# Optimization experiments

Hardware: AMD Instinct MI355X
Metric: run time of the kernel (lower is better)

The kernel has to match this reference:

```python
import jax, jax.numpy as jnp
import numpy as np

H = 56; W = 56; WS = 7; SHIFT = 3; HEADS = 6; C = 192
HD = C // HEADS; N = WS * WS; NWH = H // WS; NWW = W // WS; NW = NWH * NWW
MLP_HID = 4 * C
EPS = 1e-5


def _rel_index(ws):
    coords = np.stack(np.meshgrid(np.arange(ws), np.arange(ws), indexing='ij'))  # [2,ws,ws]
    cf = coords.reshape(2, -1)                       # [2,N]
    rc = (cf[:, :, None] - cf[:, None, :]).transpose(1, 2, 0).astype(np.int64)  # [N,N,2]
    rc[..., 0] += ws - 1
    rc[..., 1] += ws - 1
    rc[..., 0] *= 2 * ws - 1
    return rc.sum(-1)                                # [N,N]


def _attn_mask(h, w, ws, shift):
    img = np.zeros((h, w), dtype=np.float32)
    slices = (slice(0, -ws), slice(-ws, -shift), slice(-shift, None))
    cnt = 0
    for hs in slices:
        for wsl in slices:
            img[hs, wsl] = cnt
            cnt += 1
    mw = img.reshape(h // ws, ws, w // ws, ws).transpose(0, 2, 1, 3).reshape(-1, ws * ws)  # [nW,N]
    am = mw[:, None, :] - mw[:, :, None]             # [nW,N,N] (unsqueeze(1)-unsqueeze(2))
    return np.where(am != 0, np.float32(-100.0), np.float32(0.0))


REL_IDX = jnp.asarray(_rel_index(WS))
ATTN_MASK = jnp.asarray(_attn_mask(H, W, WS, SHIFT))


def _ln(x, w, b):
    m = jnp.mean(x, axis=-1, keepdims=True)
    v = jnp.mean((x - m) ** 2, axis=-1, keepdims=True)
    return (x - m) * jax.lax.rsqrt(v + EPS) * w + b


def setup_inputs() -> dict:
    key = jax.random.key(0)
    ks = jax.random.split(key, 8)
    B = 64
    s = 0.02
    return {
        'x': jax.random.normal(ks[0], (B, H * W, C), jnp.float32),
        'norm1_w': jnp.ones((C,), jnp.float32),
        'norm1_b': jnp.zeros((C,), jnp.float32),
        'qkv_w': jax.random.normal(ks[1], (C, 3 * C), jnp.float32) * s,
        'qkv_b': jnp.zeros((3 * C,), jnp.float32),
        'proj_w': jax.random.normal(ks[2], (C, C), jnp.float32) * s,
        'proj_b': jnp.zeros((C,), jnp.float32),
        'rel_bias': jax.random.normal(ks[3], ((2 * WS - 1) ** 2, HEADS), jnp.float32) * s,
        'norm2_w': jnp.ones((C,), jnp.float32),
        'norm2_b': jnp.zeros((C,), jnp.float32),
        'fc1_w': jax.random.normal(ks[4], (C, MLP_HID), jnp.float32) * s,
        'fc1_b': jnp.zeros((MLP_HID,), jnp.float32),
        'fc2_w': jax.random.normal(ks[5], (MLP_HID, C), jnp.float32) * s,
        'fc2_b': jnp.zeros((C,), jnp.float32),
    }


def reference(x, norm1_w, norm1_b, qkv_w, qkv_b, proj_w, proj_b, rel_bias,
              norm2_w, norm2_b, fc1_w, fc1_b, fc2_w, fc2_b):
    B = x.shape[0]
    shortcut = x
    h = _ln(x, norm1_w, norm1_b).reshape(B, H, W, C)
    h = jnp.roll(h, (-SHIFT, -SHIFT), axis=(1, 2))
    # window partition -> [B*nW, N, C]
    wx = h.reshape(B, NWH, WS, NWW, WS, C).transpose(0, 1, 3, 2, 4, 5).reshape(B * NW, N, C)
    qkv = (wx @ qkv_w + qkv_b).reshape(B * NW, N, 3, HEADS, HD).transpose(2, 0, 3, 1, 4)
    q, k, v = qkv[0], qkv[1], qkv[2]                 # [BnW, heads, N, hd]
    attn = jnp.einsum('bhnd,bhmd->bhnm', q, k) * (HD ** -0.5)
    bias = rel_bias[REL_IDX.reshape(-1)].reshape(N, N, HEADS).transpose(2, 0, 1)  # [heads,N,N]
    attn = attn + bias[None]
    attn = attn.reshape(B, NW, HEADS, N, N) + ATTN_MASK[None, :, None]
    attn = jax.nn.softmax(attn.reshape(B * NW, HEADS, N, N), axis=-1)
    out = jnp.einsum('bhnm,bhmd->bhnd', attn, v).transpose(0, 2, 1, 3).reshape(B * NW, N, C)
    out = out @ proj_w + proj_b
    # window reverse -> [B,H,W,C]
    out = out.reshape(B, NWH, NWW, WS, WS, C).transpose(0, 1, 3, 2, 4, 5).reshape(B, H, W, C)
    out = jnp.roll(out, (SHIFT, SHIFT), axis=(1, 2)).reshape(B, H * W, C)
    x = shortcut + out
    h2 = _ln(x, norm2_w, norm2_b)
    h2 = jax.nn.gelu(h2 @ fc1_w + fc1_b, approximate=False)
    h2 = h2 @ fc2_w + fc2_b
    return x + h2
```

## Files before the change

kernel.cpp:

```cpp
#include <hip/hip_runtime.h>
#include <hip/hip_bf16.h>
#include <math.h>

typedef __bf16 bf16;
typedef bf16  bf16x4 __attribute__((ext_vector_type(4)));
typedef bf16  bf16x8 __attribute__((ext_vector_type(8)));
typedef float f32x4  __attribute__((ext_vector_type(4)));

#define CD 192
#define NHEADS 6

__device__ __forceinline__ bf16x8 ld_frag(const bf16* p, int r0, int k0, int ld) {
  const int l = threadIdx.x & 63;
  return *reinterpret_cast<const bf16x8*>(p + (r0 + (l & 15)) * ld + (k0 + 8 * (l >> 4)));
}

__device__ __forceinline__ f32x4 mfma16(bf16x8 a, bf16x8 b, f32x4 c) {
  return __builtin_amdgcn_mfma_f32_16x16x32_bf16(a, b, c, 0, 0, 0);
}

__device__ __forceinline__ float gelu_f(float v) {
  const float e = __expf(-1.5957691216057308f * (v + 0.044715f * v * v * v));
  return v * __builtin_amdgcn_rcpf(1.f + e);
}

__global__ void prep_pack(const float* __restrict__ src, bf16* __restrict__ dst, int K, int N) {
  const int t = blockIdx.x * 256 + threadIdx.x;
  const int ktiles = K >> 5;
  const int total = (N >> 4) * ktiles * 64;
  if (t >= total) return;
  const int l  = t & 63;
  const int r  = t >> 6;
  const int kt = r % ktiles;
  const int ng = r / ktiles;
  const int n  = ng * 16 + (l & 15);
  const int k0 = kt * 32 + 8 * (l >> 4);
  bf16x8 v;
  #pragma unroll
  for (int j = 0; j < 8; ++j) v[j] = (bf16)src[(size_t)(k0 + j) * N + n];
  *(reinterpret_cast<bf16x8*>(dst) + t) = v;
}

__global__ void prep_bm(const float* __restrict__ relb, float* __restrict__ bm) {
  const int idx = blockIdx.x * 256 + threadIdx.x;
  if (idx >= 4 * 6 * 64 * 64) return;
  const int k = idx & 63;
  const int r = (idx >> 6) & 63;
  const int h = (idx >> 12) % 6;
  const int c = idx / (4096 * 6);
  float v = -3000.f;
  if (r < 49 && k < 49) {
    const int rh = r / 7, rw = r % 7, kh = k / 7, kw = k % 7;
    const int crh = (c & 2) ? (rh < 4 ? 1 : 2) : 0;
    const int crw = (c & 1) ? (rw < 4 ? 1 : 2) : 0;
    const int ckh = (c & 2) ? (kh < 4 ? 1 : 2) : 0;
    const int ckw = (c & 1) ? (kw < 4 ? 1 : 2) : 0;
    const float mask = (crh == ckh && crw == ckw) ? 0.f : -100.f;
    v = relb[((rh - kh + 6) * 13 + (rw - kw + 6)) * 6 + h] + mask;
  }
  bm[idx] = v;
}

__global__ __launch_bounds__(768, 1)
void swin_attn_kernel(const float* __restrict__ x,
                      const float* __restrict__ n1w, const float* __restrict__ n1b,
                      const bf16* __restrict__ wqf, const float* __restrict__ qkvb,
                      const bf16* __restrict__ wpf, const float* __restrict__ projb,
                      const float* __restrict__ bm,
                      float* __restrict__ out)
{
  __shared__ alignas(16) bf16 sQ[NHEADS][64 * 40];
  __shared__ alignas(16) bf16 sK[NHEADS][64 * 40];
  __shared__ alignas(16) bf16 sVT[NHEADS][32 * 72];
  __shared__ alignas(16) bf16 sU[NHEADS * 64 * 72];

  const int l    = threadIdx.x & 63;
  const int wv   = threadIdx.x >> 6;
  const int h    = wv >> 1;
  const int half = wv & 1;
  const int r0w  = half * 32;
  const int b  = blockIdx.x >> 6;
  const int wi = blockIdx.x & 63;
  const int wh = wi >> 3, ww = wi & 7;
  const int cw = ((wh == 7) ? 2 : 0) + ((ww == 7) ? 1 : 0);

  bf16* sA = sU;

  {
    const float w0 = n1w[l], w1 = n1w[l + 64], w2 = n1w[l + 128];
    const float c0 = n1b[l], c1 = n1b[l + 64], c2 = n1b[l + 128];
    float v0a[5], v1a[5], v2a[5];
    #pragma unroll
    for (int it = 0; it < 5; ++it) {
      const int t = wv + it * 12;
      if (t < 49) {
        const int th = t / 7, tw = t - 7 * th;
        const int ho = (wh * 7 + th + 3) % 56;
        const int wo = (ww * 7 + tw + 3) % 56;
        const float* xr = x + ((size_t)b * 3136 + ho * 56 + wo) * CD;
        v0a[it] = xr[l]; v1a[it] = xr[l + 64]; v2a[it] = xr[l + 128];
      }
    }
    #pragma unroll
    for (int it = 0; it < 5; ++it) {
      const int t = wv + it * 12;
      if (t < 49) {
        const float v0 = v0a[it], v1 = v1a[it], v2 = v2a[it];
        float s  = v0 + v1 + v2;
        float ss = v0 * v0 + v1 * v1 + v2 * v2;
        #pragma unroll
        for (int off = 32; off; off >>= 1) { s += __shfl_xor(s, off); ss += __shfl_xor(ss, off); }
        const float mean = s * (1.f / 192.f);
        const float inv  = rsqrtf(ss * (1.f / 192.f) - mean * mean + 1e-5f);
        sA[t * 200 + l]       = (bf16)((v0 - mean) * inv * w0 + c0);
        sA[t * 200 + l + 64]  = (bf16)((v1 - mean) * inv * w1 + c1);
        sA[t * 200 + l + 128] = (bf16)((v2 - mean) * inv * w2 + c2);
      }
    }
    for (int i = threadIdx.x; i < 15 * 200; i += 768) sA[49 * 200 + i] = (bf16)0.f;
  }
  __syncthreads();

  float bmreg[2][4][4];
  {
    const float* bmb = bm + ((size_t)(cw * 6 + h) << 12) + (l & 15);
    #pragma unroll
    for (int mt = 0; mt < 2; ++mt)
      #pragma unroll
      for (int i = 0; i < 4; ++i) {
        const int r = r0w + mt * 16 + (l >> 4) * 4 + i;
        #pragma unroll
        for (int nt = 0; nt < 4; ++nt)
          bmreg[mt][i][nt] = bmb[r * 64 + nt * 16];
      }
  }

  {
    const bf16x8* bq = reinterpret_cast<const bf16x8*>(wqf) + l;
    f32x4 acc[6][2] = {};
    #pragma unroll
    for (int ks = 0; ks < 6; ++ks) {
      const int k0 = ks * 32;
      bf16x8 af0 = ld_frag(sA, r0w,      k0, 200);
      bf16x8 af1 = ld_frag(sA, r0w + 16, k0, 200);
      #pragma unroll
      for (int nt = 0; nt < 6; ++nt) {
        const int ng = (nt >> 1) * 12 + h * 2 + (nt & 1);
        const bf16x8 bfr = bq[(ng * 6 + ks) * 64];
        acc[nt][0] = mfma16(af0, bfr, acc[nt][0]);
        acc[nt][1] = mfma16(af1, bfr, acc[nt][1]);
      }
    }
    #pragma unroll
    for (int nt = 0; nt < 6; ++nt) {
      const int which = nt >> 1;
      const int c = (nt & 1) * 16 + (l & 15);
      const float bias = qkvb[which * 192 + h * 32 + c];
      #pragma unroll
      for (int mt = 0; mt < 2; ++mt) {
        const int rb = r0w + mt * 16 + (l >> 4) * 4;
        if (which == 2) {
          bf16x4 pv;
          #pragma unroll
          for (int i = 0; i < 4; ++i) pv[i] = (bf16)(acc[nt][mt][i] + bias);
          *reinterpret_cast<bf16x4*>(&sVT[h][c * 72 + rb]) = pv;
        } else if (which == 0) {
          #pragma unroll
          for (int i = 0; i < 4; ++i)
            sQ[h][(rb + i) * 40 + c] = (bf16)((acc[nt][mt][i] + bias) * 0.17677669529663689f);
        } else {
          #pragma unroll
          for (int i = 0; i < 4; ++i)
            sK[h][(rb + i) * 40 + c] = (bf16)(acc[nt][mt][i] + bias);
        }
      }
    }
  }
  __syncthreads();

  bf16* sP = sU + h * (64 * 72);
  {
    f32x4 sc[2][4] = {};
    bf16x8 qf0 = ld_frag(sQ[h], r0w,      0, 40);
    bf16x8 qf1 = ld_frag(sQ[h], r0w + 16, 0, 40);
    #pragma unroll
    for (int nt = 0; nt < 4; ++nt) {
      const bf16x8 kf = ld_frag(sK[h], nt * 16, 0, 40);
      sc[0][nt] = mfma16(qf0, kf, sc[0][nt]);
      sc[1][nt] = mfma16(qf1, kf, sc[1][nt]);
    }
    #pragma unroll
    for (int mt = 0; mt < 2; ++mt)
      #pragma unroll
      for (int i = 0; i < 4; ++i) {
        const int r = r0w + mt * 16 + (l >> 4) * 4 + i;
        float p[4], sum = 0.f;
        #pragma unroll
        for (int nt = 0; nt < 4; ++nt) {
          p[nt] = __expf(sc[mt][nt][i] + bmreg[mt][i][nt]);
          sum += p[nt];
        }
        #pragma unroll
        for (int off = 1; off < 16; off <<= 1) sum += __shfl_xor(sum, off);
        const float isum = __builtin_amdgcn_rcpf(sum);
        #pragma unroll
        for (int nt = 0; nt < 4; ++nt)
          sP[r * 72 + nt * 16 + (l & 15)] = (bf16)(p[nt] * isum);
      }
  }

  f32x4 o[2][2] = {};
  #pragma unroll
  for (int ks = 0; ks < 2; ++ks) {
    const int k0 = ks * 32;
    bf16x8 pf0 = ld_frag(sP, r0w,      k0, 72);
    bf16x8 pf1 = ld_frag(sP, r0w + 16, k0, 72);
    #pragma unroll
    for (int nt = 0; nt < 2; ++nt) {
      const bf16x8 vf = ld_frag(sVT[h], nt * 16, k0, 72);
      o[0][nt] = mfma16(pf0, vf, o[0][nt]);
      o[1][nt] = mfma16(pf1, vf, o[1][nt]);
    }
  }
  __syncthreads();
  {
    bf16* sAO = sU;
    #pragma unroll
    for (int nt = 0; nt < 2; ++nt) {
      const int c = h * 32 + nt * 16 + (l & 15);
      #pragma unroll
      for (int mt = 0; mt < 2; ++mt)
        #pragma unroll
        for (int i = 0; i < 4; ++i) {
          const int r = r0w + mt * 16 + (l >> 4) * 4 + i;
          sAO[r * 200 + c] = (bf16)o[mt][nt][i];
        }
    }
  }
  __syncthreads();

  f32x4 po[2][2] = {};
  {
    const bf16* sAO = sU;
    const bf16x8* bp = reinterpret_cast<const bf16x8*>(wpf) + l;
    #pragma unroll
    for (int ks = 0; ks < 6; ++ks) {
      const int k0 = ks * 32;
      bf16x8 af0 = ld_frag(sAO, r0w,      k0, 200);
      bf16x8 af1 = ld_frag(sAO, r0w + 16, k0, 200);
      #pragma unroll
      for (int nt = 0; nt < 2; ++nt) {
        const bf16x8 bfr = bp[((h * 2 + nt) * 6 + ks) * 64];
        po[0][nt] = mfma16(af0, bfr, po[0][nt]);
        po[1][nt] = mfma16(af1, bfr, po[1][nt]);
      }
    }
  }
  __syncthreads();

  {
    bf16* sPO = sU;
    #pragma unroll
    for (int nt = 0; nt < 2; ++nt) {
      const int c = h * 32 + nt * 16 + (l & 15);
      const float bias = projb[c];
      #pragma unroll
      for (int mt = 0; mt < 2; ++mt)
        #pragma unroll
        for (int i = 0; i < 4; ++i) {
          const int r = r0w + mt * 16 + (l >> 4) * 4 + i;
          sPO[r * 200 + c] = (bf16)(po[mt][nt][i] + bias);
        }
    }
  }
  __syncthreads();

  {
    const bf16* sPO = sU;
    float x0a[5], x1a[5], x2a[5];
    size_t basea[5];
    #pragma unroll
    for (int it = 0; it < 5; ++it) {
      const int r = wv + it * 12;
      if (r < 49) {
        const int th = r / 7, tw = r - 7 * th;
        const int ho = (wh * 7 + th + 3) % 56;
        const int wo = (ww * 7 + tw + 3) % 56;
        const size_t base = ((size_t)b * 3136 + ho * 56 + wo) * CD;
        basea[it] = base;
        x0a[it] = x[base + l]; x1a[it] = x[base + l + 64]; x2a[it] = x[base + l + 128];
      }
    }
    #pragma unroll
    for (int it = 0; it < 5; ++it) {
      const int r = wv + it * 12;
      if (r < 49) {
        const size_t base = basea[it];
        out[base + l]       = (float)sPO[r * 200 + l]       + x0a[it];
        out[base + l + 64]  = (float)sPO[r * 200 + l + 64]  + x1a[it];
        out[base + l + 128] = (float)sPO[r * 200 + l + 128] + x2a[it];
      }
    }
  }
}

__global__ __launch_bounds__(512, 6)
void swin_mlp_kernel(const float* __restrict__ n2w, const float* __restrict__ n2b,
                     const bf16* __restrict__ w1f, const float* __restrict__ fb1,
                     const bf16* __restrict__ w2f, const float* __restrict__ fb2,
                     float* __restrict__ io)
{
  __shared__ alignas(16) bf16 sA[64 * 200];
  __shared__ alignas(16) bf16 sH[2][64 * 72];
  const int l  = threadIdx.x & 63;
  const int wv = threadIdx.x >> 6;
  const int wr = wv & 1;
  const int wc = wv >> 1;
  const size_t t0 = (size_t)blockIdx.x * 64;

  {
    const float w0 = n2w[l], w1 = n2w[l + 64], w2 = n2w[l + 128];
    const float c0 = n2b[l], c1 = n2b[l + 64], c2 = n2b[l + 128];
    for (int t = wv; t < 64; t += 8) {
      const float* xr = io + (t0 + t) * CD;
      float v0 = xr[l], v1 = xr[l + 64], v2 = xr[l + 128];
      float s  = v0 + v1 + v2;
      float ss = v0 * v0 + v1 * v1 + v2 * v2;
      #pragma unroll
      for (int off = 32; off; off >>= 1) { s += __shfl_xor(s, off); ss += __shfl_xor(ss, off); }
      const float mean = s * (1.f / 192.f);
      const float inv  = rsqrtf(ss * (1.f / 192.f) - mean * mean + 1e-5f);
      sA[t * 200 + l]       = (bf16)((v0 - mean) * inv * w0 + c0);
      sA[t * 200 + l + 64]  = (bf16)((v1 - mean) * inv * w1 + c1);
      sA[t * 200 + l + 128] = (bf16)((v2 - mean) * inv * w2 + c2);
    }
  }
  __syncthreads();

  f32x4 oacc[2][3] = {};
  const bf16x8* w1p = reinterpret_cast<const bf16x8*>(w1f) + l;
  const bf16x8* w2p = reinterpret_cast<const bf16x8*>(w2f) + l;

  for (int kc = 0; kc < 12; ++kc) {
    bf16* hb = sH[kc & 1];
    f32x4 acc[2] = {};
    {
      bf16x8 b1[6];
      const bf16x8* b1p = w1p + ((kc * 4 + wc) * 6) * 64;
      #pragma unroll
      for (int ks = 0; ks < 6; ++ks) b1[ks] = b1p[ks * 64];

      #pragma unroll
      for (int ks = 0; ks < 6; ++ks) {
        const int k0 = ks * 32;
        bf16x8 af0 = ld_frag(sA, wr * 32,      k0, 200);
        bf16x8 af1 = ld_frag(sA, wr * 32 + 16, k0, 200);
        acc[0] = mfma16(af0, b1[ks], acc[0]);
        acc[1] = mfma16(af1, b1[ks], acc[1]);
      }
    }

    bf16x8 b2[6];
    #pragma unroll
    for (int ks = 0; ks < 2; ++ks)
      #pragma unroll
      for (int nt = 0; nt < 3; ++nt)
        b2[ks * 3 + nt] = w2p[((wc * 3 + nt) * 24 + kc * 2 + ks) * 64];

    {
      const int col = wc * 16 + (l & 15);
      const float bias = fb1[kc * 64 + col];
      #pragma unroll
      for (int mt = 0; mt < 2; ++mt)
        #pragma unroll
        for (int i = 0; i < 4; ++i) {
          const int r = wr * 32 + mt * 16 + (l >> 4) * 4 + i;
          hb[r * 72 + col] = (bf16)gelu_f(acc[mt][i] + bias);
        }
    }
    __syncthreads();
    #pragma unroll
    for (int ks = 0; ks < 2; ++ks) {
      const int k0 = ks * 32;
      bf16x8 af0 = ld_frag(hb, wr * 32,      k0, 72);
      bf16x8 af1 = ld_frag(hb, wr * 32 + 16, k0, 72);
      #pragma unroll
      for (int nt = 0; nt < 3; ++nt) {
        oacc[0][nt] = mfma16(af0, b2[ks * 3 + nt], oacc[0][nt]);
        oacc[1][nt] = mfma16(af1, b2[ks * 3 + nt], oacc[1][nt]);
      }
    }
  }

  #pragma unroll
  for (int nt = 0; nt < 3; ++nt) {
    const int col = wc * 48 + nt * 16 + (l & 15);
    const float bias = fb2[col];
    #pragma unroll
    for (int mt = 0; mt < 2; ++mt)
      #pragma unroll
      for (int i = 0; i < 4; ++i) {
        const int r = wr * 32 + mt * 16 + (l >> 4) * 4 + i;
        const size_t idx = (t0 + r) * CD + col;
        __builtin_nontemporal_store(oacc[mt][nt][i] + bias + io[idx], &io[idx]);
      }
  }
}

extern "C" void kernel_launch(void* const* d_in, const int* in_sizes, int n_in,
                              void* d_out, int out_size, void* d_ws, size_t ws_size,
                              hipStream_t stream) {
  const float* x     = (const float*)d_in[0];
  const float* n1w   = (const float*)d_in[1];
  const float* n1b   = (const float*)d_in[2];
  const float* qkvw  = (const float*)d_in[3];
  const float* qkvb  = (const float*)d_in[4];
  const float* projw = (const float*)d_in[5];
  const float* projb = (const float*)d_in[6];
  const float* relb  = (const float*)d_in[7];
  const float* n2w   = (const float*)d_in[8];
  const float* n2b   = (const float*)d_in[9];
  const float* f1w   = (const float*)d_in[10];
  const float* f1b   = (const float*)d_in[11];
  const float* f2w   = (const float*)d_in[12];
  const float* f2b   = (const float*)d_in[13];

  char* ws = (char*)d_ws;
  bf16*  wqf = (bf16*)(ws + 0);
  bf16*  wpf = (bf16*)(ws + 221184);
  bf16*  w1f = (bf16*)(ws + 294912);
  bf16*  w2f = (bf16*)(ws + 589824);
  float* bm  = (float*)(ws + 884736);

  prep_pack<<<(36 * 6 * 64 + 255) / 256, 256, 0, stream>>>(qkvw, wqf, 192, 576);
  prep_pack<<<(12 * 6 * 64 + 255) / 256, 256, 0, stream>>>(projw, wpf, 192, 192);
  prep_pack<<<(48 * 6 * 64 + 255) / 256, 256, 0, stream>>>(f1w, w1f, 192, 768);
  prep_pack<<<(12 * 24 * 64 + 255) / 256, 256, 0, stream>>>(f2w, w2f, 768, 192);
  prep_bm<<<(4 * 6 * 64 * 64 + 255) / 256, 256, 0, stream>>>(relb, bm);

  swin_attn_kernel<<<4096, 768, 0, stream>>>(x, n1w, n1b, wqf, qkvb, wpf, projb, bm, (float*)d_out);
  swin_mlp_kernel<<<3136, 512, 0, stream>>>(n2w, n2b, w1f, f1b, w2f, f2b, (float*)d_out);
}
```

Before: 487.1 us.

## Repartition QKV and proj GEMMs across waves; keep residual x in registers

The QKV and projection GEMMs are re-tiled so that each of the 12 waves owns a column slice across all 64 rows, rather than a head and half-rows pair. This cuts redundant weight-fragment loads per wave, since each B fragment now feeds four MFMAs instead of two. The residual x values loaded for LayerNorm stay in registers until the final store, which removes the second global read of x. The cost is higher register pressure, because 15 floats plus 5 size_t offsets stay live across the whole kernel, and that could reduce occupancy.

```diff
diff --git a/kernel.cpp b/kernel.cpp
--- a/kernel.cpp
+++ b/kernel.cpp
@@ -86,10 +86,9 @@
 
   bf16* sA = sU;
 
-  {
-    const float w0 = n1w[l], w1 = n1w[l + 64], w2 = n1w[l + 128];
-    const float c0 = n1b[l], c1 = n1b[l + 64], c2 = n1b[l + 128];
-    float v0a[5], v1a[5], v2a[5];
+  float xv0[5], xv1[5], xv2[5];
+  size_t basea[5];
+  {
     #pragma unroll
     for (int it = 0; it < 5; ++it) {
       const int t = wv + it * 12;
@@ -97,15 +96,18 @@
         const int th = t / 7, tw = t - 7 * th;
         const int ho = (wh * 7 + th + 3) % 56;
         const int wo = (ww * 7 + tw + 3) % 56;
-        const float* xr = x + ((size_t)b * 3136 + ho * 56 + wo) * CD;
-        v0a[it] = xr[l]; v1a[it] = xr[l + 64]; v2a[it] = xr[l + 128];
-      }
-    }
+        const size_t base = ((size_t)b * 3136 + ho * 56 + wo) * CD;
+        basea[it] = base;
+        xv0[it] = x[base + l]; xv1[it] = x[base + l + 64]; xv2[it] = x[base + l + 128];
+      }
+    }
+    const float w0 = n1w[l], w1 = n1w[l + 64], w2 = n1w[l + 128];
+    const float c0 = n1b[l], c1 = n1b[l + 64], c2 = n1b[l + 128];
     #pragma unroll
     for (int it = 0; it < 5; ++it) {
       const int t = wv + it * 12;
       if (t < 49) {
-        const float v0 = v0a[it], v1 = v1a[it], v2 = v2a[it];
+        const float v0 = xv0[it], v1 = xv1[it], v2 = xv2[it];
         float s  = v0 + v1 + v2;
         float ss = v0 * v0 + v1 * v1 + v2 * v2;
         #pragma unroll
@@ -137,41 +139,45 @@
 
   {
     const bf16x8* bq = reinterpret_cast<const bf16x8*>(wqf) + l;
-    f32x4 acc[6][2] = {};
+    const int cs = wv;
+    f32x4 acc[3][4] = {};
     #pragma unroll
     for (int ks = 0; ks < 6; ++ks) {
       const int k0 = ks * 32;
-      bf16x8 af0 = ld_frag(sA, r0w,      k0, 200);
-      bf16x8 af1 = ld_frag(sA, r0w + 16, k0, 200);
-      #pragma unroll
-      for (int nt = 0; nt < 6; ++nt) {
-        const int ng = (nt >> 1) * 12 + h * 2 + (nt & 1);
-        const bf16x8 bfr = bq[(ng * 6 + ks) * 64];
-        acc[nt][0] = mfma16(af0, bfr, acc[nt][0]);
-        acc[nt][1] = mfma16(af1, bfr, acc[nt][1]);
-      }
-    }
-    #pragma unroll
-    for (int nt = 0; nt < 6; ++nt) {
-      const int which = nt >> 1;
-      const int c = (nt & 1) * 16 + (l & 15);
-      const float bias = qkvb[which * 192 + h * 32 + c];
-      #pragma unroll
-      for (int mt = 0; mt < 2; ++mt) {
-        const int rb = r0w + mt * 16 + (l >> 4) * 4;
+      bf16x8 af[4];
+      #pragma unroll
+      for (int mt = 0; mt < 4; ++mt) af[mt] = ld_frag(sA, mt * 16, k0, 200);
+      #pragma unroll
+      for (int nt = 0; nt < 3; ++nt) {
+        const bf16x8 bfr = bq[((cs * 3 + nt) * 6 + ks) * 64];
+        #pragma unroll
+        for (int mt = 0; mt < 4; ++mt) acc[nt][mt] = mfma16(af[mt], bfr, acc[nt][mt]);
+      }
+    }
+    #pragma unroll
+    for (int nt = 0; nt < 3; ++nt) {
+      const int col0 = cs * 48 + nt * 16;
+      const int which = col0 / 192;
+      const int rem   = col0 - which * 192;
+      const int hh    = rem >> 5;
+      const int cc    = (rem & 31) + (l & 15);
+      const float bias = qkvb[col0 + (l & 15)];
+      #pragma unroll
+      for (int mt = 0; mt < 4; ++mt) {
+        const int rb = mt * 16 + (l >> 4) * 4;
         if (which == 2) {
           bf16x4 pv;
           #pragma unroll
           for (int i = 0; i < 4; ++i) pv[i] = (bf16)(acc[nt][mt][i] + bias);
-          *reinterpret_cast<bf16x4*>(&sVT[h][c * 72 + rb]) = pv;
+          *reinterpret_cast<bf16x4*>(&sVT[hh][cc * 72 + rb]) = pv;
         } else if (which == 0) {
           #pragma unroll
           for (int i = 0; i < 4; ++i)
-            sQ[h][(rb + i) * 40 + c] = (bf16)((acc[nt][mt][i] + bias) * 0.17677669529663689f);
+            sQ[hh][(rb + i) * 40 + cc] = (bf16)((acc[nt][mt][i] + bias) * 0.17677669529663689f);
         } else {
           #pragma unroll
           for (int i = 0; i < 4; ++i)
-            sK[h][(rb + i) * 40 + c] = (bf16)(acc[nt][mt][i] + bias);
+            sK[hh][(rb + i) * 40 + cc] = (bf16)(acc[nt][mt][i] + bias);
         }
       }
     }
@@ -239,20 +245,18 @@
   }
   __syncthreads();
 
-  f32x4 po[2][2] = {};
+  f32x4 po[4] = {};
   {
     const bf16* sAO = sU;
     const bf16x8* bp = reinterpret_cast<const bf16x8*>(wpf) + l;
     #pragma unroll
     for (int ks = 0; ks < 6; ++ks) {
       const int k0 = ks * 32;
-      bf16x8 af0 = ld_frag(sAO, r0w,      k0, 200);
-      bf16x8 af1 = ld_frag(sAO, r0w + 16, k0, 200);
-      #pragma unroll
-      for (int nt = 0; nt < 2; ++nt) {
-        const bf16x8 bfr = bp[((h * 2 + nt) * 6 + ks) * 64];
-        po[0][nt] = mfma16(af0, bfr, po[0][nt]);
-        po[1][nt] = mfma16(af1, bfr, po[1][nt]);
+      const bf16x8 bfr = bp[(wv * 6 + ks) * 64];
+      #pragma unroll
+      for (int mt = 0; mt < 4; ++mt) {
+        bf16x8 af = ld_frag(sAO, mt * 16, k0, 200);
+        po[mt] = mfma16(af, bfr, po[mt]);
       }
     }
   }
@@ -260,45 +264,28 @@
 
   {
     bf16* sPO = sU;
-    #pragma unroll
-    for (int nt = 0; nt < 2; ++nt) {
-      const int c = h * 32 + nt * 16 + (l & 15);
-      const float bias = projb[c];
-      #pragma unroll
-      for (int mt = 0; mt < 2; ++mt)
-        #pragma unroll
-        for (int i = 0; i < 4; ++i) {
-          const int r = r0w + mt * 16 + (l >> 4) * 4 + i;
-          sPO[r * 200 + c] = (bf16)(po[mt][nt][i] + bias);
-        }
-    }
+    const int c = wv * 16 + (l & 15);
+    const float bias = projb[c];
+    #pragma unroll
+    for (int mt = 0; mt < 4; ++mt)
+      #pragma unroll
+      for (int i = 0; i < 4; ++i) {
+        const int r = mt * 16 + (l >> 4) * 4 + i;
+        sPO[r * 200 + c] = (bf16)(po[mt][i] + bias);
+      }
   }
   __syncthreads();
 
   {
     const bf16* sPO = sU;
-    float x0a[5], x1a[5], x2a[5];
-    size_t basea[5];
-    #pragma unroll
-    for (int it = 0; it < 5; ++it) {
-      const int r = wv + it * 12;
-      if (r < 49) {
-        const int th = r / 7, tw = r - 7 * th;
-        const int ho = (wh * 7 + th + 3) % 56;
-        const int wo = (ww * 7 + tw + 3) % 56;
-        const size_t base = ((size_t)b * 3136 + ho * 56 + wo) * CD;
-        basea[it] = base;
-        x0a[it] = x[base + l]; x1a[it] = x[base + l + 64]; x2a[it] = x[base + l + 128];
-      }
-    }
     #pragma unroll
     for (int it = 0; it < 5; ++it) {
       const int r = wv + it * 12;
       if (r < 49) {
         const size_t base = basea[it];
-        out[base + l]       = (float)sPO[r * 200 + l]       + x0a[it];
-        out[base + l + 64]  = (float)sPO[r * 200 + l + 64]  + x1a[it];
-        out[base + l + 128] = (float)sPO[r * 200 + l + 128] + x2a[it];
+        out[base + l]       = (float)sPO[r * 200 + l]       + xv0[it];
+        out[base + l + 64]  = (float)sPO[r * 200 + l + 64]  + xv1[it];
+        out[base + l + 128] = (float)sPO[r * 200 + l + 128] + xv2[it];
       }
     }
   }
```

After: 475.8 us. 2.3% less time.
